# Performance work log

Measured on AMD Instinct MI355X. Metric: run time of the kernel, lower is better.

## Reference

```python
import jax, jax.numpy as jnp
import numpy as np

NUM_CHANNELS = 256
NUM_HEADS = 4
HEAD_DIM = 64


def setup_inputs() -> dict:
    key = jax.random.key(0)
    k1, k2, k3, k4, k5 = jax.random.split(key, 5)
    C, H, D = NUM_CHANNELS, NUM_HEADS, HEAD_DIM
    x = jax.random.normal(k1, (8, C, 32, 32), dtype=jnp.float32)
    # projection: Linear(C -> H*D*3); stored as (in, out)
    Wp = jax.random.normal(k2, (C, H * D * 3), dtype=jnp.float32) / np.sqrt(C)
    bp = jnp.zeros((H * D * 3,), dtype=jnp.float32)
    # output: Linear(H*D -> C)
    Wo = jax.random.normal(k3, (H * D, C), dtype=jnp.float32) / np.sqrt(H * D)
    bo = jnp.zeros((C,), dtype=jnp.float32)
    return {"x": x, "Wp": Wp, "bp": bp, "Wo": Wo, "bo": bo}


def reference(x, Wp, bp, Wo, bo):
    B, C, Hh, Ww = x.shape
    Nh, Dh = NUM_HEADS, HEAD_DIM
    scale = Dh ** (-0.5)
    # (B, C, H, W) -> (B, N, C)
    xs = x.reshape(B, C, Hh * Ww).transpose(0, 2, 1)
    # QKV projection -> (B, N, heads, 3*head_dim)
    qkv = (xs @ Wp + bp).reshape(B, -1, Nh, 3 * Dh)
    q, k, v = jnp.split(qkv, 3, axis=-1)  # each (B, N, heads, head_dim)
    # NOTE: original forward never applies self.norm, so no GroupNorm here.
    attn = jnp.einsum('bihd,bjhd->bijh', q, k) * scale  # (B, N, N, heads)
    attn = jax.nn.softmax(attn, axis=2)
    res = jnp.einsum('bijh,bjhd->bihd', attn, v)  # (B, N, heads, head_dim)
    res = res.reshape(B, -1, Nh * Dh)
    res = res @ Wo + bo  # (B, N, C)
    out = res + xs
    return out.transpose(0, 2, 1).reshape(B, C, Hh, Ww)
```

## Files before the change

kernel.cpp:

```cpp
#include <hip/hip_runtime.h>

typedef __attribute__((ext_vector_type(8))) short short8;
typedef __attribute__((ext_vector_type(4))) float f32x4;
typedef __attribute__((ext_vector_type(16))) float f32x16;
typedef __attribute__((ext_vector_type(2))) unsigned int u32x2;

#define NB 8
#define NC 256
#define NH 4
#define ND 64
#define NN 1024
#define OC3 768

__device__ __forceinline__ unsigned short f2bf(float f) {
  union { float f; unsigned int u; } a;
  a.f = f;
  unsigned int r = a.u + 0x7fffu + ((a.u >> 16) & 1u);
  return (unsigned short)(r >> 16);
}

__device__ __forceinline__ unsigned int pkbf(float lo, float hi) {
  union { float f; unsigned int u; } a, b;
  a.f = lo; b.f = hi;
  return __builtin_amdgcn_perm(b.u + 0x8000u, a.u + 0x8000u, 0x07060302u);
}

typedef const unsigned int __attribute__((address_space(1)))* gp_t;
typedef unsigned int __attribute__((address_space(3)))* lp_t;
__device__ __forceinline__ void glds16(const unsigned short* g, unsigned short* l) {
  __builtin_amdgcn_global_load_lds((gp_t)g, (lp_t)l, 16, 0, 0);
}

__global__ __launch_bounds__(256) void trans_all(
    const float* __restrict__ x, const float* __restrict__ Wp,
    const float* __restrict__ Wo, unsigned short* __restrict__ xs,
    unsigned short* __restrict__ WpT, unsigned short* __restrict__ WoT) {
  __shared__ float T[64][65];
  int z = blockIdx.z;
  const float* in; unsigned short* out; int R, S;
  if (z < 8) { in = x + (size_t)z * NC * NN; out = xs + (size_t)z * NC * NN; R = NC; S = NN; }
  else if (z == 8) { if (blockIdx.x >= 12) return; in = Wp; out = WpT; R = NC; S = OC3; }
  else { if (blockIdx.x >= 4) return; in = Wo; out = WoT; R = NC; S = NC; }
  int s0 = blockIdx.x * 64, r0 = blockIdx.y * 64;
  int t = threadIdx.x;
  {
    int ri = t >> 2, sb = t & 3;
    const float* p = in + (size_t)(r0 + ri) * S + s0 + sb * 16;
    float4 v0 = *(const float4*)(p);
    float4 v1 = *(const float4*)(p + 4);
    float4 v2 = *(const float4*)(p + 8);
    float4 v3 = *(const float4*)(p + 12);
    float vv[16] = {v0.x, v0.y, v0.z, v0.w, v1.x, v1.y, v1.z, v1.w,
                    v2.x, v2.y, v2.z, v2.w, v3.x, v3.y, v3.z, v3.w};
#pragma unroll
    for (int e = 0; e < 16; ++e) T[ri][sb * 16 + e] = vv[e];
  }
  __syncthreads();
  {
    int so = t >> 2, rb = t & 3;
    union { unsigned short us[16]; uint4 v[2]; } pk;
#pragma unroll
    for (int e = 0; e < 16; ++e) pk.us[e] = f2bf(T[rb * 16 + e][so]);
    uint4* dst = (uint4*)(out + (size_t)(s0 + so) * R + r0 + rb * 16);
    dst[0] = pk.v[0];
    dst[1] = pk.v[1];
  }
}

__global__ __launch_bounds__(256) void gemm_qkv(
    const unsigned short* __restrict__ xs, const unsigned short* __restrict__ WpT,
    const float* __restrict__ bp,
    unsigned short* __restrict__ Qf, unsigned short* __restrict__ Kf,
    unsigned short* __restrict__ Vf) {
  __shared__ __attribute__((aligned(16))) unsigned short Al[64 * 72];
  __shared__ __attribute__((aligned(16))) unsigned short Bl[64 * 72];
  int nt = blockIdx.x, mt = blockIdx.y;
  int t = threadIdx.x, w = t >> 6, l = t & 63, q = l >> 4, c = l & 15;
  f32x4 acc[4] = {{0, 0, 0, 0}, {0, 0, 0, 0}, {0, 0, 0, 0}, {0, 0, 0, 0}};
  const unsigned short* Arow = xs + (size_t)(mt * 64) * NC;
  const unsigned short* Brow = WpT + (size_t)(nt * 64) * NC;
  for (int k0 = 0; k0 < NC; k0 += 64) {
    __syncthreads();
#pragma unroll
    for (int it = 0; it < 2; ++it) {
      int u = t + it * 256;
      int row = u >> 3, kb = u & 7;
      *(uint4*)&Al[row * 72 + kb * 8] = *(const uint4*)(Arow + (size_t)row * NC + k0 + kb * 8);
      *(uint4*)&Bl[row * 72 + kb * 8] = *(const uint4*)(Brow + (size_t)row * NC + k0 + kb * 8);
    }
    __syncthreads();
#pragma unroll
    for (int ks = 0; ks < 2; ++ks) {
      short8 a = *(const short8*)&Al[(w * 16 + c) * 72 + ks * 32 + q * 8];
#pragma unroll
      for (int ct = 0; ct < 4; ++ct) {
        short8 b = *(const short8*)&Bl[(ct * 16 + c) * 72 + ks * 32 + q * 8];
        acc[ct] = __builtin_amdgcn_mfma_f32_16x16x32_bf16(a, b, acc[ct], 0, 0, 0);
      }
    }
  }
  int o0 = nt * 64;
  int h = o0 / 192, rem = o0 % 192;
  int b = mt >> 4, itl = mt & 15;
  int bh = b * NH + h;
  size_t rbase = (size_t)bh * 65536;
#pragma unroll
  for (int ct = 0; ct < 4; ++ct) {
    float bias = bp[o0 + ct * 16 + c];
#pragma unroll
    for (int r = 0; r < 4; ++r) acc[ct][r] += bias;
  }
  if (rem < 128) {
    unsigned short* dst = (rem == 0) ? Qf : Kf;
    float sc = (rem == 0) ? 0.18033688011112042f : 1.0f;
    int tile32 = itl * 2 + (w >> 1);
    int lpb = (c >> 3) * 32 + (w & 1) * 16 + q * 4;
    size_t tb = rbase + (size_t)tile32 * 2048 + (size_t)(c & 7);
#pragma unroll
    for (int ct = 0; ct < 4; ++ct)
#pragma unroll
      for (int r = 0; r < 4; ++r)
        dst[tb + (size_t)ct * 512 + (size_t)((lpb + r) * 8)] = f2bf(acc[ct][r] * sc);
  } else {
#pragma unroll
    for (int ct = 0; ct < 4; ++ct) {
      int f = itl * 8 + (ct >> 1) * 4 + w;
      int lp = (q >> 1) * 32 + (ct & 1) * 16 + c;
      size_t off = rbase + (size_t)f * 512 + (size_t)(lp * 8 + (q & 1) * 4);
      uint2 pk2 = {pkbf(acc[ct][0], acc[ct][1]), pkbf(acc[ct][2], acc[ct][3])};
      *(uint2*)&Vf[off] = pk2;
    }
  }
}

__global__ __launch_bounds__(256) void attn(
    const unsigned short* __restrict__ Qf, const unsigned short* __restrict__ Kf,
    const unsigned short* __restrict__ Vf, unsigned short* __restrict__ O) {
  __shared__ __attribute__((aligned(16))) unsigned short Kl[2][4096];
  __shared__ __attribute__((aligned(16))) unsigned short Vl[2][4096];
  int B = blockIdx.x;
  int bh = (B & 7) + 8 * ((B >> 3) & 3);
  int it = B >> 5;
  int t = threadIdx.x, w = t >> 6, l = t & 63;
  int jh = w & 1, isub = w >> 1;
  const unsigned short* Qt = Qf + (size_t)bh * 65536 + (size_t)(it * 2 + isub) * 2048;
  short8 bq[4];
#pragma unroll
  for (int dc = 0; dc < 4; ++dc) bq[dc] = *(const short8*)(Qt + dc * 512 + l * 8);
  const unsigned short* Kt = Kf + (size_t)bh * 65536;
  const unsigned short* Vt = Vf + (size_t)bh * 65536;

#pragma unroll
  for (int m = 0; m < 2; ++m) {
    int ch = (m * 4 + w) * 512;
    glds16(Kt + ch + l * 8, &Kl[0][ch]);
    glds16(Vt + ch + l * 8, &Vl[0][ch]);
  }

  float lsum = 0.f;
  f32x16 oacc0 = {0, 0, 0, 0, 0, 0, 0, 0, 0, 0, 0, 0, 0, 0, 0, 0};
  f32x16 oacc1 = {0, 0, 0, 0, 0, 0, 0, 0, 0, 0, 0, 0, 0, 0, 0, 0};
  int p = 0;
  for (int jt = 0; jt < 16; ++jt) {
    __syncthreads();
    if (jt < 15) {
      const unsigned short* ksn = Kt + (size_t)(jt + 1) * 4096;
      const unsigned short* vsn = Vt + (size_t)(jt + 1) * 4096;
#pragma unroll
      for (int m = 0; m < 2; ++m) {
        int ch = (m * 4 + w) * 512;
        glds16(ksn + ch + l * 8, &Kl[p ^ 1][ch]);
        glds16(vsn + ch + l * 8, &Vl[p ^ 1][ch]);
      }
    }
    f32x16 sT = {0, 0, 0, 0, 0, 0, 0, 0, 0, 0, 0, 0, 0, 0, 0, 0};
#pragma unroll
    for (int dc = 0; dc < 4; ++dc) {
      short8 ka = *(const short8*)&Kl[p][(jh * 4 + dc) * 512 + l * 8];
      sT = __builtin_amdgcn_mfma_f32_32x32x16_bf16(ka, bq[dc], sT, 0, 0, 0);
    }
    float e_[16];
#pragma unroll
    for (int rg = 0; rg < 16; ++rg) {
      e_[rg] = __builtin_amdgcn_exp2f(sT[rg]);
      lsum += e_[rg];
    }
#pragma unroll
    for (int kk = 0; kk < 2; ++kk) {
      unsigned int x1 = pkbf(e_[kk * 8 + 0], e_[kk * 8 + 1]);
      unsigned int x2 = pkbf(e_[kk * 8 + 2], e_[kk * 8 + 3]);
      unsigned int y1 = pkbf(e_[kk * 8 + 4], e_[kk * 8 + 5]);
      unsigned int y2 = pkbf(e_[kk * 8 + 6], e_[kk * 8 + 7]);
      u32x2 r1 = __builtin_amdgcn_permlane32_swap(x1, y1, false, false);
      u32x2 r2 = __builtin_amdgcn_permlane32_swap(x2, y2, false, false);
      union { unsigned int u[4]; short8 s; } pa;
      pa.u[0] = r1.x; pa.u[1] = r2.x; pa.u[2] = r1.y; pa.u[3] = r2.y;
      int kc = jh * 2 + kk;
      short8 v0 = *(const short8*)&Vl[p][kc * 512 + l * 8];
      short8 v1 = *(const short8*)&Vl[p][(4 + kc) * 512 + l * 8];
      oacc0 = __builtin_amdgcn_mfma_f32_32x32x16_bf16(pa.s, v0, oacc0, 0, 0, 0);
      oacc1 = __builtin_amdgcn_mfma_f32_32x32x16_bf16(pa.s, v1, oacc1, 0, 0, 0);
    }
    p ^= 1;
  }
  lsum += __shfl_xor(lsum, 32);
  __syncthreads();
  float* LF = (float*)&Kl[0][0];
  float* LS = (float*)&Vl[0][0];
  int pr = w >> 1;
  if (w & 1) {
#pragma unroll
    for (int rg = 0; rg < 16; ++rg) {
      LF[pr * 2048 + rg * 64 + l] = oacc0[rg];
      LF[pr * 2048 + 1024 + rg * 64 + l] = oacc1[rg];
    }
    LS[pr * 64 + l] = lsum;
  }
  __syncthreads();
  if (!(w & 1)) {
    lsum += LS[pr * 64 + l];
    float inv = 1.0f / lsum;
    int hi = l >> 5, cl = l & 31;
    int b = bh >> 2, h = bh & 3;
    int i0 = it * 64 + isub * 32;
#pragma unroll
    for (int rg = 0; rg < 16; ++rg) {
      int ri = (rg & 3) + 8 * (rg >> 2) + 4 * hi;
      float invr = __shfl(inv, ri, 64);
      float o0v = oacc0[rg] + LF[pr * 2048 + rg * 64 + l];
      float o1v = oacc1[rg] + LF[pr * 2048 + 1024 + rg * 64 + l];
      size_t base = ((size_t)b * NN + (i0 + ri)) * NC + h * ND + cl;
      O[base] = f2bf(o0v * invr);
      O[base + 32] = f2bf(o1v * invr);
    }
  }
}

__global__ __launch_bounds__(256) void gemm_out(
    const unsigned short* __restrict__ O, const unsigned short* __restrict__ WoT,
    const float* __restrict__ bo, const float* __restrict__ x,
    float* __restrict__ out) {
  __shared__ __attribute__((aligned(16))) unsigned short Al[64 * 72];
  __shared__ __attribute__((aligned(16))) unsigned short Bl[64 * 72];
  __shared__ float Tl[64 * 65];
  int nt = blockIdx.x, mt = blockIdx.y;
  int t = threadIdx.x, w = t >> 6, l = t & 63, q = l >> 4, c = l & 15;
  f32x4 acc[4] = {{0, 0, 0, 0}, {0, 0, 0, 0}, {0, 0, 0, 0}, {0, 0, 0, 0}};
  const unsigned short* Arow = O + (size_t)(mt * 64) * NC;
  const unsigned short* Brow = WoT + (size_t)(nt * 64) * NC;
  for (int k0 = 0; k0 < NC; k0 += 64) {
    __syncthreads();
#pragma unroll
    for (int it = 0; it < 2; ++it) {
      int u = t + it * 256;
      int row = u >> 3, kb = u & 7;
      *(uint4*)&Al[row * 72 + kb * 8] = *(const uint4*)(Arow + (size_t)row * NC + k0 + kb * 8);
      *(uint4*)&Bl[row * 72 + kb * 8] = *(const uint4*)(Brow + (size_t)row * NC + k0 + kb * 8);
    }
    __syncthreads();
#pragma unroll
    for (int ks = 0; ks < 2; ++ks) {
      short8 a = *(const short8*)&Al[(w * 16 + c) * 72 + ks * 32 + q * 8];
#pragma unroll
      for (int ct = 0; ct < 4; ++ct) {
        short8 b = *(const short8*)&Bl[(ct * 16 + c) * 72 + ks * 32 + q * 8];
        acc[ct] = __builtin_amdgcn_mfma_f32_16x16x32_bf16(a, b, acc[ct], 0, 0, 0);
      }
    }
  }
#pragma unroll
  for (int ct = 0; ct < 4; ++ct) {
    float bias = bo[nt * 64 + ct * 16 + c];
#pragma unroll
    for (int r = 0; r < 4; ++r)
      Tl[(ct * 16 + c) * 65 + w * 16 + q * 4 + r] = acc[ct][r] + bias;
  }
  __syncthreads();
  int b = (mt * 64) >> 10, n0 = (mt * 64) & 1023;
  int cl = t >> 2, nb = t & 3;
  float v[16];
#pragma unroll
  for (int e = 0; e < 16; ++e) v[e] = Tl[cl * 65 + nb * 16 + e];
  size_t base = ((size_t)(b * NC + nt * 64 + cl)) * NN + n0 + nb * 16;
#pragma unroll
  for (int g = 0; g < 4; ++g) {
    float4 xv = *(const float4*)(x + base + g * 4);
    float4 ov;
    ov.x = v[g * 4 + 0] + xv.x;
    ov.y = v[g * 4 + 1] + xv.y;
    ov.z = v[g * 4 + 2] + xv.z;
    ov.w = v[g * 4 + 3] + xv.w;
    *(float4*)(out + base + g * 4) = ov;
  }
}

extern "C" void kernel_launch(void* const* d_in, const int* in_sizes, int n_in,
                              void* d_out, int out_size, void* d_ws, size_t ws_size,
                              hipStream_t stream) {
  const float* x = (const float*)d_in[0];
  const float* Wp = (const float*)d_in[1];
  const float* bp = (const float*)d_in[2];
  const float* Wo = (const float*)d_in[3];
  const float* bo = (const float*)d_in[4];
  float* out = (float*)d_out;
  char* ws = (char*)d_ws;
  unsigned short* xs  = (unsigned short*)(ws);
  unsigned short* WpT = (unsigned short*)(ws + 4194304);
  unsigned short* WoT = (unsigned short*)(ws + 4587520);
  unsigned short* Qfr = (unsigned short*)(ws + 4718592);
  unsigned short* Kfr = (unsigned short*)(ws + 8912896);
  unsigned short* Vfr = (unsigned short*)(ws + 13107200);
  unsigned short* Ob  = (unsigned short*)(ws + 17301504);

  hipLaunchKernelGGL(trans_all, dim3(16, 4, 10), dim3(256), 0, stream,
                     x, Wp, Wo, xs, WpT, WoT);
  hipLaunchKernelGGL(gemm_qkv, dim3(12, 128), dim3(256), 0, stream, xs, WpT, bp,
                     Qfr, Kfr, Vfr);
  hipLaunchKernelGGL(attn, dim3(512), dim3(256), 0, stream, Qfr, Kfr, Vfr, Ob);
  hipLaunchKernelGGL(gemm_out, dim3(4, 128), dim3(256), 0, stream, Ob, WoT, bo, x, out);
}
```

Baseline: 105.7 us.

## Fuse fp32 transpose and bf16 conversion into GEMM loads, drop transpose kernel

Removes the separate trans_all kernel and makes gemm_qkv and gemm_out read fp32 x, Wp and Wo directly. They convert to bf16 and transpose into LDS while loading each tile. Block indices are also remapped into a 1D grid that groups 8 M-tiles per N-tile for better L2 reuse. This saves one launch and the bf16 staging round-trip through global memory. In exchange the GEMMs load twice the bytes, repeat the conversion in every block, and use scattered 4-byte LDS stores.

```diff
diff --git a/kernel.cpp b/kernel.cpp
--- a/kernel.cpp
+++ b/kernel.cpp
@@ -31,62 +31,42 @@
   __builtin_amdgcn_global_load_lds((gp_t)g, (lp_t)l, 16, 0, 0);
 }
 
-__global__ __launch_bounds__(256) void trans_all(
+__global__ __launch_bounds__(256) void gemm_qkv(
     const float* __restrict__ x, const float* __restrict__ Wp,
-    const float* __restrict__ Wo, unsigned short* __restrict__ xs,
-    unsigned short* __restrict__ WpT, unsigned short* __restrict__ WoT) {
-  __shared__ float T[64][65];
-  int z = blockIdx.z;
-  const float* in; unsigned short* out; int R, S;
-  if (z < 8) { in = x + (size_t)z * NC * NN; out = xs + (size_t)z * NC * NN; R = NC; S = NN; }
-  else if (z == 8) { if (blockIdx.x >= 12) return; in = Wp; out = WpT; R = NC; S = OC3; }
-  else { if (blockIdx.x >= 4) return; in = Wo; out = WoT; R = NC; S = NC; }
-  int s0 = blockIdx.x * 64, r0 = blockIdx.y * 64;
-  int t = threadIdx.x;
-  {
-    int ri = t >> 2, sb = t & 3;
-    const float* p = in + (size_t)(r0 + ri) * S + s0 + sb * 16;
-    float4 v0 = *(const float4*)(p);
-    float4 v1 = *(const float4*)(p + 4);
-    float4 v2 = *(const float4*)(p + 8);
-    float4 v3 = *(const float4*)(p + 12);
-    float vv[16] = {v0.x, v0.y, v0.z, v0.w, v1.x, v1.y, v1.z, v1.w,
-                    v2.x, v2.y, v2.z, v2.w, v3.x, v3.y, v3.z, v3.w};
-#pragma unroll
-    for (int e = 0; e < 16; ++e) T[ri][sb * 16 + e] = vv[e];
-  }
-  __syncthreads();
-  {
-    int so = t >> 2, rb = t & 3;
-    union { unsigned short us[16]; uint4 v[2]; } pk;
-#pragma unroll
-    for (int e = 0; e < 16; ++e) pk.us[e] = f2bf(T[rb * 16 + e][so]);
-    uint4* dst = (uint4*)(out + (size_t)(s0 + so) * R + r0 + rb * 16);
-    dst[0] = pk.v[0];
-    dst[1] = pk.v[1];
-  }
-}
-
-__global__ __launch_bounds__(256) void gemm_qkv(
-    const unsigned short* __restrict__ xs, const unsigned short* __restrict__ WpT,
     const float* __restrict__ bp,
     unsigned short* __restrict__ Qf, unsigned short* __restrict__ Kf,
     unsigned short* __restrict__ Vf) {
   __shared__ __attribute__((aligned(16))) unsigned short Al[64 * 72];
   __shared__ __attribute__((aligned(16))) unsigned short Bl[64 * 72];
-  int nt = blockIdx.x, mt = blockIdx.y;
+  int B = blockIdx.x;
+  int nt = (B >> 3) % 12;
+  int mt = (B & 7) + 8 * (B / 96);
   int t = threadIdx.x, w = t >> 6, l = t & 63, q = l >> 4, c = l & 15;
+  int cp = (t >> 3) * 2, np = t & 7;
   f32x4 acc[4] = {{0, 0, 0, 0}, {0, 0, 0, 0}, {0, 0, 0, 0}, {0, 0, 0, 0}};
-  const unsigned short* Arow = xs + (size_t)(mt * 64) * NC;
-  const unsigned short* Brow = WpT + (size_t)(nt * 64) * NC;
+  int b = mt >> 4, itl = mt & 15;
+  int nl0 = itl * 64;
+  int o0 = nt * 64;
+  const float* xb = x + ((size_t)b * NC) * NN + nl0 + np * 8;
+  const float* wb = Wp + o0 + np * 8;
   for (int k0 = 0; k0 < NC; k0 += 64) {
     __syncthreads();
-#pragma unroll
-    for (int it = 0; it < 2; ++it) {
-      int u = t + it * 256;
-      int row = u >> 3, kb = u & 7;
-      *(uint4*)&Al[row * 72 + kb * 8] = *(const uint4*)(Arow + (size_t)row * NC + k0 + kb * 8);
-      *(uint4*)&Bl[row * 72 + kb * 8] = *(const uint4*)(Brow + (size_t)row * NC + k0 + kb * 8);
+    const float* pa0 = xb + (size_t)(k0 + cp) * NN;
+    const float* pa1 = pa0 + NN;
+    float4 a00 = *(const float4*)pa0, a01 = *(const float4*)(pa0 + 4);
+    float4 a10 = *(const float4*)pa1, a11 = *(const float4*)(pa1 + 4);
+    const float* pb0 = wb + (size_t)(k0 + cp) * OC3;
+    const float* pb1 = pb0 + OC3;
+    float4 b00 = *(const float4*)pb0, b01 = *(const float4*)(pb0 + 4);
+    float4 b10 = *(const float4*)pb1, b11 = *(const float4*)(pb1 + 4);
+    float a0v[8] = {a00.x, a00.y, a00.z, a00.w, a01.x, a01.y, a01.z, a01.w};
+    float a1v[8] = {a10.x, a10.y, a10.z, a10.w, a11.x, a11.y, a11.z, a11.w};
+    float b0v[8] = {b00.x, b00.y, b00.z, b00.w, b01.x, b01.y, b01.z, b01.w};
+    float b1v[8] = {b10.x, b10.y, b10.z, b10.w, b11.x, b11.y, b11.z, b11.w};
+#pragma unroll
+    for (int e = 0; e < 8; ++e) {
+      *(unsigned int*)&Al[(np * 8 + e) * 72 + cp] = pkbf(a0v[e], a1v[e]);
+      *(unsigned int*)&Bl[(np * 8 + e) * 72 + cp] = pkbf(b0v[e], b1v[e]);
     }
     __syncthreads();
 #pragma unroll
@@ -94,14 +74,12 @@
       short8 a = *(const short8*)&Al[(w * 16 + c) * 72 + ks * 32 + q * 8];
 #pragma unroll
       for (int ct = 0; ct < 4; ++ct) {
-        short8 b = *(const short8*)&Bl[(ct * 16 + c) * 72 + ks * 32 + q * 8];
-        acc[ct] = __builtin_amdgcn_mfma_f32_16x16x32_bf16(a, b, acc[ct], 0, 0, 0);
+        short8 bb = *(const short8*)&Bl[(ct * 16 + c) * 72 + ks * 32 + q * 8];
+        acc[ct] = __builtin_amdgcn_mfma_f32_16x16x32_bf16(a, bb, acc[ct], 0, 0, 0);
       }
     }
   }
-  int o0 = nt * 64;
   int h = o0 / 192, rem = o0 % 192;
-  int b = mt >> 4, itl = mt & 15;
   int bh = b * NH + h;
   size_t rbase = (size_t)bh * 65536;
 #pragma unroll
@@ -237,17 +215,21 @@
 }
 
 __global__ __launch_bounds__(256) void gemm_out(
-    const unsigned short* __restrict__ O, const unsigned short* __restrict__ WoT,
+    const unsigned short* __restrict__ O, const float* __restrict__ Wo,
     const float* __restrict__ bo, const float* __restrict__ x,
     float* __restrict__ out) {
   __shared__ __attribute__((aligned(16))) unsigned short Al[64 * 72];
   __shared__ __attribute__((aligned(16))) unsigned short Bl[64 * 72];
   __shared__ float Tl[64 * 65];
-  int nt = blockIdx.x, mt = blockIdx.y;
+  int B = blockIdx.x;
+  int nt = (B >> 3) & 3;
+  int mt = (B & 7) + 8 * (B >> 5);
   int t = threadIdx.x, w = t >> 6, l = t & 63, q = l >> 4, c = l & 15;
+  int cp = (t >> 3) * 2, np = t & 7;
   f32x4 acc[4] = {{0, 0, 0, 0}, {0, 0, 0, 0}, {0, 0, 0, 0}, {0, 0, 0, 0}};
+  int o0 = nt * 64;
   const unsigned short* Arow = O + (size_t)(mt * 64) * NC;
-  const unsigned short* Brow = WoT + (size_t)(nt * 64) * NC;
+  const float* wb = Wo + o0 + np * 8;
   for (int k0 = 0; k0 < NC; k0 += 64) {
     __syncthreads();
 #pragma unroll
@@ -255,22 +237,30 @@
       int u = t + it * 256;
       int row = u >> 3, kb = u & 7;
       *(uint4*)&Al[row * 72 + kb * 8] = *(const uint4*)(Arow + (size_t)row * NC + k0 + kb * 8);
-      *(uint4*)&Bl[row * 72 + kb * 8] = *(const uint4*)(Brow + (size_t)row * NC + k0 + kb * 8);
-    }
+    }
+    const float* pb0 = wb + (size_t)(k0 + cp) * NC;
+    const float* pb1 = pb0 + NC;
+    float4 b00 = *(const float4*)pb0, b01 = *(const float4*)(pb0 + 4);
+    float4 b10 = *(const float4*)pb1, b11 = *(const float4*)(pb1 + 4);
+    float b0v[8] = {b00.x, b00.y, b00.z, b00.w, b01.x, b01.y, b01.z, b01.w};
+    float b1v[8] = {b10.x, b10.y, b10.z, b10.w, b11.x, b11.y, b11.z, b11.w};
+#pragma unroll
+    for (int e = 0; e < 8; ++e)
+      *(unsigned int*)&Bl[(np * 8 + e) * 72 + cp] = pkbf(b0v[e], b1v[e]);
     __syncthreads();
 #pragma unroll
     for (int ks = 0; ks < 2; ++ks) {
       short8 a = *(const short8*)&Al[(w * 16 + c) * 72 + ks * 32 + q * 8];
 #pragma unroll
       for (int ct = 0; ct < 4; ++ct) {
-        short8 b = *(const short8*)&Bl[(ct * 16 + c) * 72 + ks * 32 + q * 8];
-        acc[ct] = __builtin_amdgcn_mfma_f32_16x16x32_bf16(a, b, acc[ct], 0, 0, 0);
+        short8 bb = *(const short8*)&Bl[(ct * 16 + c) * 72 + ks * 32 + q * 8];
+        acc[ct] = __builtin_amdgcn_mfma_f32_16x16x32_bf16(a, bb, acc[ct], 0, 0, 0);
       }
     }
   }
 #pragma unroll
   for (int ct = 0; ct < 4; ++ct) {
-    float bias = bo[nt * 64 + ct * 16 + c];
+    float bias = bo[o0 + ct * 16 + c];
 #pragma unroll
     for (int r = 0; r < 4; ++r)
       Tl[(ct * 16 + c) * 65 + w * 16 + q * 4 + r] = acc[ct][r] + bias;
@@ -281,7 +271,7 @@
   float v[16];
 #pragma unroll
   for (int e = 0; e < 16; ++e) v[e] = Tl[cl * 65 + nb * 16 + e];
-  size_t base = ((size_t)(b * NC + nt * 64 + cl)) * NN + n0 + nb * 16;
+  size_t base = ((size_t)(b * NC + o0 + cl)) * NN + n0 + nb * 16;
 #pragma unroll
   for (int g = 0; g < 4; ++g) {
     float4 xv = *(const float4*)(x + base + g * 4);
@@ -304,18 +294,13 @@
   const float* bo = (const float*)d_in[4];
   float* out = (float*)d_out;
   char* ws = (char*)d_ws;
-  unsigned short* xs  = (unsigned short*)(ws);
-  unsigned short* WpT = (unsigned short*)(ws + 4194304);
-  unsigned short* WoT = (unsigned short*)(ws + 4587520);
-  unsigned short* Qfr = (unsigned short*)(ws + 4718592);
-  unsigned short* Kfr = (unsigned short*)(ws + 8912896);
-  unsigned short* Vfr = (unsigned short*)(ws + 13107200);
-  unsigned short* Ob  = (unsigned short*)(ws + 17301504);
-
-  hipLaunchKernelGGL(trans_all, dim3(16, 4, 10), dim3(256), 0, stream,
-                     x, Wp, Wo, xs, WpT, WoT);
-  hipLaunchKernelGGL(gemm_qkv, dim3(12, 128), dim3(256), 0, stream, xs, WpT, bp,
+  unsigned short* Qfr = (unsigned short*)(ws);
+  unsigned short* Kfr = (unsigned short*)(ws + 4194304);
+  unsigned short* Vfr = (unsigned short*)(ws + 8388608);
+  unsigned short* Ob  = (unsigned short*)(ws + 12582912);
+
+  hipLaunchKernelGGL(gemm_qkv, dim3(1536), dim3(256), 0, stream, x, Wp, bp,
                      Qfr, Kfr, Vfr);
   hipLaunchKernelGGL(attn, dim3(512), dim3(256), 0, stream, Qfr, Kfr, Vfr, Ob);
-  hipLaunchKernelGGL(gemm_out, dim3(4, 128), dim3(256), 0, stream, Ob, WoT, bo, x, out);
-}
+  hipLaunchKernelGGL(gemm_out, dim3(512), dim3(256), 0, stream, Ob, Wo, bo, x, out);
+}
```

Result: slower. 112.7 us (+6.7%).

## Double-buffer QKV GEMM with direct global-to-LDS loads and 128-row tiles

Applied to the files above, without the earlier changes.

Reworks the QKV projection GEMM to use 128x64 output tiles, with each warp computing two 16-row MFMA fragments that share the B operand. K-tiles are staged into double-buffered LDS through direct global-to-LDS 16-byte loads with an XOR swizzle instead of padded rows. The next tile is prefetched while MFMAs run on the current one. The aim is to cut barrier stalls and global reload traffic. The cost is halving the grid size and doubling accumulator registers, which may reduce occupancy.

```diff
diff --git a/kernel.cpp b/kernel.cpp
--- a/kernel.cpp
+++ b/kernel.cpp
@@ -72,63 +72,90 @@
     const float* __restrict__ bp,
     unsigned short* __restrict__ Qf, unsigned short* __restrict__ Kf,
     unsigned short* __restrict__ Vf) {
-  __shared__ __attribute__((aligned(16))) unsigned short Al[64 * 72];
-  __shared__ __attribute__((aligned(16))) unsigned short Bl[64 * 72];
+  __shared__ __attribute__((aligned(16))) unsigned short Albuf[2][8192];
+  __shared__ __attribute__((aligned(16))) unsigned short Blbuf[2][4096];
   int nt = blockIdx.x, mt = blockIdx.y;
   int t = threadIdx.x, w = t >> 6, l = t & 63, q = l >> 4, c = l & 15;
-  f32x4 acc[4] = {{0, 0, 0, 0}, {0, 0, 0, 0}, {0, 0, 0, 0}, {0, 0, 0, 0}};
-  const unsigned short* Arow = xs + (size_t)(mt * 64) * NC;
-  const unsigned short* Brow = WpT + (size_t)(nt * 64) * NC;
-  for (int k0 = 0; k0 < NC; k0 += 64) {
+  f32x4 acc[2][4] = {{{0,0,0,0},{0,0,0,0},{0,0,0,0},{0,0,0,0}},
+                     {{0,0,0,0},{0,0,0,0},{0,0,0,0},{0,0,0,0}}};
+  int mbase = mt * 128, o0 = nt * 64;
+  int rsub = l >> 3, cch = l & 7;
+  int kxo = ((cch ^ rsub) << 3);
+
+  auto stage = [&](int kt, int pp) {
+    int kx = kt * 64 + kxo;
+#pragma unroll
+    for (int m = 0; m < 4; ++m) {
+      int ra = w + m * 4;
+      glds16(xs + (size_t)(mbase + ra * 8 + rsub) * NC + kx, &Albuf[pp][ra * 512]);
+    }
+#pragma unroll
+    for (int m = 0; m < 2; ++m) {
+      int rb = w + m * 4;
+      glds16(WpT + (size_t)(o0 + rb * 8 + rsub) * NC + kx, &Blbuf[pp][rb * 512]);
+    }
+  };
+
+  stage(0, 0);
+  int p = 0;
+  for (int kt = 0; kt < 4; ++kt) {
     __syncthreads();
-#pragma unroll
-    for (int it = 0; it < 2; ++it) {
-      int u = t + it * 256;
-      int row = u >> 3, kb = u & 7;
-      *(uint4*)&Al[row * 72 + kb * 8] = *(const uint4*)(Arow + (size_t)row * NC + k0 + kb * 8);
-      *(uint4*)&Bl[row * 72 + kb * 8] = *(const uint4*)(Brow + (size_t)row * NC + k0 + kb * 8);
-    }
-    __syncthreads();
+    if (kt < 3) stage(kt + 1, p ^ 1);
+    const unsigned short* Ab = &Albuf[p][0];
+    const unsigned short* Bb = &Blbuf[p][0];
 #pragma unroll
     for (int ks = 0; ks < 2; ++ks) {
-      short8 a = *(const short8*)&Al[(w * 16 + c) * 72 + ks * 32 + q * 8];
+      int chx = (((ks * 4 + q) ^ (c & 7)) << 3);
+      short8 a0 = *(const short8*)&Ab[(w * 32 + c) * 64 + chx];
+      short8 a1 = *(const short8*)&Ab[(w * 32 + 16 + c) * 64 + chx];
 #pragma unroll
       for (int ct = 0; ct < 4; ++ct) {
-        short8 b = *(const short8*)&Bl[(ct * 16 + c) * 72 + ks * 32 + q * 8];
-        acc[ct] = __builtin_amdgcn_mfma_f32_16x16x32_bf16(a, b, acc[ct], 0, 0, 0);
+        short8 bb = *(const short8*)&Bb[(ct * 16 + c) * 64 + chx];
+        acc[0][ct] = __builtin_amdgcn_mfma_f32_16x16x32_bf16(a0, bb, acc[0][ct], 0, 0, 0);
+        acc[1][ct] = __builtin_amdgcn_mfma_f32_16x16x32_bf16(a1, bb, acc[1][ct], 0, 0, 0);
       }
     }
-  }
-  int o0 = nt * 64;
+    p ^= 1;
+  }
   int h = o0 / 192, rem = o0 % 192;
-  int b = mt >> 4, itl = mt & 15;
+  int m64 = mt * 2 + (w >> 1);
+  int b = m64 >> 4, itl = m64 & 15;
   int bh = b * NH + h;
   size_t rbase = (size_t)bh * 65536;
 #pragma unroll
   for (int ct = 0; ct < 4; ++ct) {
     float bias = bp[o0 + ct * 16 + c];
 #pragma unroll
-    for (int r = 0; r < 4; ++r) acc[ct][r] += bias;
+    for (int r = 0; r < 4; ++r) { acc[0][ct][r] += bias; acc[1][ct][r] += bias; }
   }
   if (rem < 128) {
     unsigned short* dst = (rem == 0) ? Qf : Kf;
     float sc = (rem == 0) ? 0.18033688011112042f : 1.0f;
-    int tile32 = itl * 2 + (w >> 1);
-    int lpb = (c >> 3) * 32 + (w & 1) * 16 + q * 4;
-    size_t tb = rbase + (size_t)tile32 * 2048 + (size_t)(c & 7);
-#pragma unroll
-    for (int ct = 0; ct < 4; ++ct)
-#pragma unroll
-      for (int r = 0; r < 4; ++r)
-        dst[tb + (size_t)ct * 512 + (size_t)((lpb + r) * 8)] = f2bf(acc[ct][r] * sc);
+#pragma unroll
+    for (int rr = 0; rr < 2; ++rr) {
+      int wp = (w * 2 + rr) & 3;
+      int tile32 = itl * 2 + (wp >> 1);
+      int lpb = (c >> 3) * 32 + (wp & 1) * 16 + q * 4;
+      size_t tb = rbase + (size_t)tile32 * 2048 + (size_t)(c & 7);
+#pragma unroll
+      for (int ct = 0; ct < 4; ++ct)
+#pragma unroll
+        for (int r = 0; r < 4; ++r)
+          dst[tb + (size_t)ct * 512 + (size_t)((lpb + r) * 8)] = f2bf(acc[rr][ct][r] * sc);
+    }
   } else {
 #pragma unroll
-    for (int ct = 0; ct < 4; ++ct) {
-      int f = itl * 8 + (ct >> 1) * 4 + w;
-      int lp = (q >> 1) * 32 + (ct & 1) * 16 + c;
-      size_t off = rbase + (size_t)f * 512 + (size_t)(lp * 8 + (q & 1) * 4);
-      uint2 pk2 = {pkbf(acc[ct][0], acc[ct][1]), pkbf(acc[ct][2], acc[ct][3])};
-      *(uint2*)&Vf[off] = pk2;
+    for (int rr = 0; rr < 2; ++rr) {
+      int wp = (w * 2 + rr) & 3;
+#pragma unroll
+      for (int ct = 0; ct < 4; ++ct) {
+        int f = itl * 8 + (ct >> 1) * 4 + wp;
+        int lp = (q >> 1) * 32 + (ct & 1) * 16 + c;
+        size_t off = rbase + (size_t)f * 512 + (size_t)(lp * 8 + (q & 1) * 4);
+        uint2 pk2 = {pkbf(acc[rr][ct][0], acc[rr][ct][1]),
+                     pkbf(acc[rr][ct][2], acc[rr][ct][3])};
+        *(uint2*)&Vf[off] = pk2;
+      }
     }
   }
 }
@@ -314,7 +341,7 @@
 
   hipLaunchKernelGGL(trans_all, dim3(16, 4, 10), dim3(256), 0, stream,
                      x, Wp, Wo, xs, WpT, WoT);
-  hipLaunchKernelGGL(gemm_qkv, dim3(12, 128), dim3(256), 0, stream, xs, WpT, bp,
+  hipLaunchKernelGGL(gemm_qkv, dim3(12, 64), dim3(256), 0, stream, xs, WpT, bp,
                      Qfr, Kfr, Vfr);
   hipLaunchKernelGGL(attn, dim3(512), dim3(256), 0, stream, Qfr, Kfr, Vfr, Ob);
   hipLaunchKernelGGL(gemm_out, dim3(4, 128), dim3(256), 0, stream, Ob, WoT, bo, x, out);
```

Result: no change. 106.2 us (+0.5%).
